# Kernel tuning notes

Hardware: AMD Instinct MI355X
Metric: run time of the kernel (lower is better)

Reference implementation:

```python
import jax, jax.numpy as jnp
import numpy as np

B, S, D = 4, 4096, 256


def setup_inputs() -> dict:
    key = jax.random.key(0)
    ks = jax.random.split(key, 8)
    scale = 1.0 / np.sqrt(D)
    inp = {
        "q": jax.random.normal(ks[0], (B, S, D), jnp.float32),
        "k": jax.random.normal(ks[1], (B, S, D), jnp.float32),
        "v": jax.random.normal(ks[2], (B, S, D), jnp.float32),
        # additive mask: 1 where attention is disallowed (causal), broadcast over batch
        "mask": jnp.triu(jnp.ones((S, S), jnp.float32), k=1)[None, :, :],
        "Wq": jax.random.normal(ks[3], (D, D), jnp.float32) * scale,
        "bq": jnp.zeros((D,), jnp.float32),
        "Wk": jax.random.normal(ks[4], (D, D), jnp.float32) * scale,
        "bk": jnp.zeros((D,), jnp.float32),
        "Wv": jax.random.normal(ks[5], (D, D), jnp.float32) * scale,
        "bv": jnp.zeros((D,), jnp.float32),
        "Wo": jax.random.normal(ks[6], (D, D), jnp.float32) * scale,
        "bo": jnp.zeros((D,), jnp.float32),
    }
    return inp


def reference(q, k, v, mask, Wq, bq, Wk, bk, Wv, bv, Wo, bo):
    # Dense projections (Keras Dense: x @ W + b)
    qp = q @ Wq + bq  # [B,S,D]
    kp = k @ Wk + bk
    vp = v @ Wv + bv
    dk = jnp.asarray(qp.shape[-1], qp.dtype)
    # scaled dot-product attention, materialized scores as in the source
    logits = jnp.einsum("bqd,bkd->bqk", qp, kp) / jnp.sqrt(dk)  # [B,S,S]
    logits = logits + mask * (-1e9)
    attn = jax.nn.softmax(logits, axis=-1)  # [B,S,S]
    ctx = jnp.einsum("bqk,bkd->bqd", attn, vp)  # [B,S,D]
    z = ctx @ Wo + bo
    return z, attn
```

## Files before the change

kernel.cpp:

```cpp
#include <hip/hip_runtime.h>


typedef unsigned short u16;
typedef __attribute__((ext_vector_type(8))) short short8;
typedef __attribute__((ext_vector_type(4))) float f32x4;

struct __align__(8) us4 { u16 x, y, z, w; };

#define SEQ 4096
#define DIM 256

__device__ __forceinline__ u16 f2bf(float f) {
  unsigned int u = __float_as_uint(f);
  u += 0x7fffu + ((u >> 16) & 1u);
  return (u16)(u >> 16);
}
__device__ __forceinline__ float bf2f(u16 u) {
  return __uint_as_float(((unsigned int)u) << 16);
}

__device__ __forceinline__ void cp16(const void* g, void* l) {
  __builtin_amdgcn_global_load_lds((const __attribute__((address_space(1))) void*)g,
                                   (__attribute__((address_space(3))) void*)l, 16, 0, 0);
}

__global__ void k_wt(const float* __restrict__ Wq, const float* __restrict__ Wk,
                     const float* __restrict__ Wv, const float* __restrict__ Wo,
                     u16* __restrict__ wt) {
  __shared__ float t[32][33];
  const float* W = blockIdx.z == 0 ? Wq : blockIdx.z == 1 ? Wk : blockIdx.z == 2 ? Wv : Wo;
  u16* out = wt + (size_t)blockIdx.z * 65536;
  int n0 = blockIdx.x * 32, k0 = blockIdx.y * 32;
  int tx = threadIdx.x, ty = threadIdx.y;
  for (int i = 0; i < 4; i++)
    t[ty + i * 8][tx] = W[(size_t)(k0 + ty + i * 8) * 256 + n0 + tx];
  __syncthreads();
  for (int i = 0; i < 4; i++)
    out[(size_t)(n0 + ty + i * 8) * 256 + k0 + tx] = f2bf(t[tx][ty + i * 8]);
}

__global__ void k_pgemm3(const float* __restrict__ qin, const float* __restrict__ kin,
                         const float* __restrict__ vin, const u16* __restrict__ wtall,
                         const float* __restrict__ bq, const float* __restrict__ bk,
                         const float* __restrict__ bv,
                         u16* __restrict__ qp, u16* __restrict__ kp,
                         u16* __restrict__ vpt) {
  __shared__ __align__(16) char smem[34816];
  const int z = blockIdx.z;
  const float* A = z == 0 ? qin : z == 1 ? kin : vin;
  const u16* Wt = wtall + (size_t)z * 65536;
  const float* bias = z == 0 ? bq : z == 1 ? bk : bv;
  u16* outp = z == 0 ? qp : z == 1 ? kp : vpt;
  const bool TRANS = (z == 2);

  u16* Asm = (u16*)smem;
  u16* Bsm = Asm + 4096;
  u16* tb = (u16*)smem;
  const int tid = threadIdx.x;
  const int lane = tid & 63, w = tid >> 6;
  const int wr = w >> 1, wc = w & 1;
  const int quad = lane >> 4, m16 = lane & 15;
  const int m0 = blockIdx.y * 128, n0 = blockIdx.x * 128;

  f32x4 zero = {0.f, 0.f, 0.f, 0.f};
  f32x4 acc[4][4];
  for (int i = 0; i < 4; i++)
    for (int j = 0; j < 4; j++) acc[i][j] = zero;

  for (int kk = 0; kk < 8; ++kk) {
    const int k0 = kk * 32;
    for (int h = 0; h < 2; ++h) {
      int c = tid + h * 256;
      int row = c >> 2, sub = c & 3;
      cp16(Wt + (size_t)(n0 + row) * 256 + k0 + sub * 8, Bsm + c * 8);
    }
    for (int h = 0; h < 4; ++h) {
      int idx = h * 256 + tid;
      int row = idx >> 3, q4 = idx & 7;
      float4 a4 = *(const float4*)(A + (size_t)(m0 + row) * 256 + k0 + q4 * 4);
      us4 o;
      o.x = f2bf(a4.x); o.y = f2bf(a4.y); o.z = f2bf(a4.z); o.w = f2bf(a4.w);
      *(us4*)(Asm + row * 32 + q4 * 4) = o;
    }
    __syncthreads();
    short8 a[4], b[4];
    for (int i = 0; i < 4; ++i)
      a[i] = *(const short8*)(Asm + (wr * 64 + i * 16 + m16) * 32 + quad * 8);
    for (int j = 0; j < 4; ++j)
      b[j] = *(const short8*)(Bsm + (wc * 64 + j * 16 + m16) * 32 + quad * 8);
    for (int i = 0; i < 4; ++i)
      for (int j = 0; j < 4; ++j)
        acc[i][j] = __builtin_amdgcn_mfma_f32_16x16x32_bf16(a[i], b[j], acc[i][j], 0, 0, 0);
    __syncthreads();
  }

  if (!TRANS) {
    for (int j = 0; j < 4; ++j) {
      int gn = n0 + wc * 64 + j * 16 + m16;
      float bvx = bias[gn];
      for (int i = 0; i < 4; ++i) {
        int gm = m0 + wr * 64 + i * 16 + quad * 4;
        for (int r = 0; r < 4; ++r)
          outp[(size_t)(gm + r) * 256 + gn] = f2bf(acc[i][j][r] + bvx);
      }
    }
  } else {
    for (int j = 0; j < 4; ++j) {
      int cn = wc * 64 + j * 16 + m16;
      float bvx = bias[n0 + cn];
      for (int i = 0; i < 4; ++i) {
        int rm = wr * 64 + i * 16 + quad * 4;
        us4 o;
        o.x = f2bf(acc[i][j][0] + bvx); o.y = f2bf(acc[i][j][1] + bvx);
        o.z = f2bf(acc[i][j][2] + bvx); o.w = f2bf(acc[i][j][3] + bvx);
        *(us4*)(tb + cn * 136 + rm) = o;
      }
    }
    __syncthreads();
    int b = m0 >> 12, s0 = m0 & 4095;
    u16* dst = outp + ((size_t)b << 20);
    for (int it = 0; it < 8; ++it) {
      int idx = it * 256 + tid;
      int n = idx >> 4, m8 = idx & 15;
      short8 v8 = *(const short8*)(tb + n * 136 + m8 * 8);
      *(short8*)(dst + (size_t)(n0 + n) * 4096 + s0 + m8 * 8) = v8;
    }
  }
}

__global__ void __launch_bounds__(256, 3) k_qk(const u16* __restrict__ qp,
                                               const u16* __restrict__ kp,
                                               u16* __restrict__ eb,
                                               float* __restrict__ attn,
                                               float* __restrict__ ps) {
  int lin = blockIdx.x + (blockIdx.y << 5) + (blockIdx.z << 10);
  int wid = (lin & 7) * 512 + (lin >> 3);
  const int kt = wid & 31, qt = (wid >> 5) & 31, bz = wid >> 10;
  const int tid = threadIdx.x;
  const int q0 = qt * 128, k0t = kt * 128;

  if (kt > qt) {
    float* attnb = attn + ((size_t)bz << 24);
    f32x4 z4 = {0.f, 0.f, 0.f, 0.f};
    for (int s = 0; s < 16; ++s) {
      int idx = tid + s * 256;
      int row = idx >> 5, c4 = idx & 31;
      __builtin_nontemporal_store(z4,
          (f32x4*)(attnb + (size_t)(q0 + row) * 4096 + k0t + c4 * 4));
    }
    return;
  }

  __shared__ __align__(16) char smem[34816];
  u16* A_lds = (u16*)smem;
  u16* B_lds = A_lds + 8192;
  u16* epi = (u16*)smem;
  __shared__ float prow[2][128];

  const int lane = tid & 63, w = tid >> 6;
  const int wr = w >> 1, wc = w & 1;
  const int quad = lane >> 4, m16 = lane & 15;
  const u16* Ab = qp + ((size_t)bz << 20);
  const u16* Bb = kp + ((size_t)bz << 20);

  short8 arg[4], brg[4];
  const int sc = tid & 7;
  int srow[4], soff[4];
  for (int t = 0; t < 4; ++t) {
    srow[t] = (t * 256 + tid) >> 3;
    soff[t] = srow[t] * 64 + ((((sc << 4) ^ ((srow[t] & 7) << 4))) >> 1);
  }

  auto stage_load = [&](int kk) {
    const int k0 = kk * 64;
    for (int t = 0; t < 4; ++t) {
      arg[t] = *(const short8*)(Ab + (size_t)(q0 + srow[t]) * 256 + k0 + sc * 8);
      brg[t] = *(const short8*)(Bb + (size_t)(k0t + srow[t]) * 256 + k0 + sc * 8);
    }
  };
  auto stage_write = [&]() {
    for (int t = 0; t < 4; ++t) {
      *(short8*)(A_lds + soff[t]) = arg[t];
      *(short8*)(B_lds + soff[t]) = brg[t];
    }
  };

  f32x4 zero = {0.f, 0.f, 0.f, 0.f};
  f32x4 acc[4][4];
  for (int i = 0; i < 4; i++)
    for (int j = 0; j < 4; j++) acc[i][j] = zero;

  stage_load(0);
  stage_write();
  __syncthreads();

  for (int kk = 0; kk < 4; ++kk) {
    if (kk + 1 < 4) stage_load(kk + 1);
    for (int ks = 0; ks < 2; ++ks) {
      short8 a[4], b[4];
      for (int i = 0; i < 4; ++i) {
        int row = wr * 64 + i * 16 + m16;
        int xb = (ks * 64 + quad * 16) ^ ((row & 7) << 4);
        a[i] = *(const short8*)(A_lds + row * 64 + (xb >> 1));
      }
      for (int j = 0; j < 4; ++j) {
        int n = wc * 64 + j * 16 + m16;
        int xb = (ks * 64 + quad * 16) ^ ((n & 7) << 4);
        b[j] = *(const short8*)(B_lds + n * 64 + (xb >> 1));
      }
      for (int i = 0; i < 4; ++i)
        for (int j = 0; j < 4; ++j)
          acc[i][j] = __builtin_amdgcn_mfma_f32_16x16x32_bf16(a[i], b[j], acc[i][j], 0, 0, 0);
    }
    __syncthreads();
    if (kk + 1 < 4) {
      stage_write();
      __syncthreads();
    }
  }

  float rs[4][4];
  for (int i = 0; i < 4; i++)
    for (int r = 0; r < 4; r++) rs[i][r] = 0.f;
  for (int i = 0; i < 4; ++i) {
    int gq = q0 + wr * 64 + i * 16 + quad * 4;
    for (int j = 0; j < 4; ++j) {
      int gk = k0t + wc * 64 + j * 16 + m16;
      for (int r = 0; r < 4; ++r) {
        float e = (gk <= gq + r) ? __expf(acc[i][j][r] * 0.0625f) : 0.f;
        acc[i][j][r] = e;
        rs[i][r] += e;
      }
    }
  }
  for (int off = 1; off < 16; off <<= 1)
    for (int i = 0; i < 4; ++i)
      for (int r = 0; r < 4; ++r) rs[i][r] += __shfl_xor(rs[i][r], off, 64);
  if (m16 == 0)
    for (int i = 0; i < 4; ++i)
      for (int r = 0; r < 4; ++r)
        prow[wc][wr * 64 + i * 16 + quad * 4 + r] = rs[i][r];

  for (int i = 0; i < 4; ++i)
    for (int j = 0; j < 4; ++j) {
      int rl = wr * 64 + i * 16 + quad * 4;
      int cl = wc * 64 + j * 16 + m16;
      for (int r = 0; r < 4; ++r) epi[(rl + r) * 136 + cl] = f2bf(acc[i][j][r]);
    }
  __syncthreads();

  u16* ebt = eb + ((size_t)bz * 528 + (size_t)(qt * (qt + 1) / 2 + kt)) * 16384;
  for (int it = 0; it < 8; ++it) {
    int idx = it * 256 + tid;
    int row = idx >> 4, m8 = idx & 15;
    short8 v8 = *(const short8*)(epi + row * 136 + m8 * 8);
    *(short8*)(ebt + row * 128 + m8 * 8) = v8;
  }
  if (tid < 128)
    ps[(size_t)(bz * 32 + kt) * 4096 + q0 + tid] = prow[0][tid] + prow[1][tid];
}

__global__ void __launch_bounds__(256) k_pv2(const u16* __restrict__ eb,
                                             const u16* __restrict__ vpt,
                                             const float* __restrict__ ps,
                                             float* __restrict__ attn,
                                             float* __restrict__ ctxf) {
  int lin = blockIdx.x + (blockIdx.y << 3) + (blockIdx.z << 8);
  int wid = (lin & 7) * 128 + (lin >> 3);
  const int nh = wid & 1, kg = (wid >> 1) & 3;
  const int qt = (wid >> 3) & 31, bz = wid >> 8;
  const int nt_lo = (kg * (qt + 1)) >> 2;
  const int nt_hi = ((kg + 1) * (qt + 1)) >> 2;
  if (nt_lo >= nt_hi) return;

  __shared__ u16 A_lds[2][128 * 64];
  __shared__ u16 B_lds[2][128 * 64];
  __shared__ float inv_lds[128];

  const int tid = threadIdx.x;
  const int lane = tid & 63, w = tid >> 6;
  const int wr = w >> 1, wc = w & 1;
  const int quad = lane >> 4, m16 = lane & 15;
  const int q0 = qt * 128;
  const u16* ebq = eb + ((size_t)bz * 528 + (size_t)(qt * (qt + 1) / 2)) * 16384;
  float* attnb = attn + ((size_t)bz << 24);
  const u16* vb = vpt + ((size_t)bz << 20) + (size_t)nh * 128 * 4096;

  if (tid < 128) {
    float s = 0.f;
    for (int kt = 0; kt <= qt; ++kt)
      s += ps[(size_t)(bz * 32 + kt) * 4096 + q0 + tid];
    inv_lds[tid] = 1.f / s;
  }

  short8 arg[4], brg[4];
  const int sc = tid & 7;
  int srow[4], soff[4];
  for (int t = 0; t < 4; ++t) {
    srow[t] = (t * 256 + tid) >> 3;
    soff[t] = srow[t] * 64 + ((((sc << 4) ^ ((srow[t] & 7) << 4))) >> 1);
  }

  auto stage_load = [&](int hh) {
    int t0 = nt_lo + (hh >> 1), h = hh & 1;
    const u16* tile = ebq + (size_t)t0 * 16384 + h * 64;
    int kt0 = t0 * 128 + h * 64;
    for (int t = 0; t < 4; ++t) {
      arg[t] = *(const short8*)(tile + srow[t] * 128 + sc * 8);
      brg[t] = *(const short8*)(vb + (size_t)srow[t] * 4096 + kt0 + sc * 8);
    }
  };
  auto stage_write = [&](int buf) {
    for (int t = 0; t < 4; ++t) {
      *(short8*)(A_lds[buf] + soff[t]) = arg[t];
      *(short8*)(B_lds[buf] + soff[t]) = brg[t];
    }
  };

  const int khalves = (nt_hi - nt_lo) * 2;
  stage_load(0);
  stage_write(0);
  __syncthreads();

  f32x4 zero = {0.f, 0.f, 0.f, 0.f};
  f32x4 acc[4][4];
  for (int i = 0; i < 4; i++)
    for (int j = 0; j < 4; j++) acc[i][j] = zero;

  for (int hh = 0; hh < khalves; ++hh) {
    const int buf = hh & 1;
    if (hh + 1 < khalves) stage_load(hh + 1);

    for (int p = 0; p < 4; ++p) {
      int idx = p * 256 + tid;
      int rl = idx >> 3, c8 = idx & 7;
      int lb = rl * 64 + ((((c8 << 4) ^ ((rl & 7) << 4))) >> 1);
      short8 e8 = *(const short8*)(A_lds[buf] + lb);
      float ivr = inv_lds[rl];
      f32x4 lo, hi;
      for (int t = 0; t < 4; ++t) lo[t] = bf2f((u16)e8[t]) * ivr;
      for (int t = 0; t < 4; ++t) hi[t] = bf2f((u16)e8[t + 4]) * ivr;
      int kcol = (nt_lo + (hh >> 1)) * 128 + (hh & 1) * 64 + (c8 << 3);
      float* dst = attnb + (size_t)(q0 + rl) * 4096 + kcol;
      __builtin_nontemporal_store(lo, (f32x4*)dst);
      __builtin_nontemporal_store(hi, (f32x4*)(dst + 4));
    }

    for (int ks = 0; ks < 2; ++ks) {
      short8 a[4], b[4];
      for (int i = 0; i < 4; ++i) {
        int row = wr * 64 + i * 16 + m16;
        int xb = (ks * 64 + quad * 16) ^ ((row & 7) << 4);
        a[i] = *(const short8*)(A_lds[buf] + row * 64 + (xb >> 1));
      }
      for (int j = 0; j < 4; ++j) {
        int n = wc * 64 + j * 16 + m16;
        int xb = (ks * 64 + quad * 16) ^ ((n & 7) << 4);
        b[j] = *(const short8*)(B_lds[buf] + n * 64 + (xb >> 1));
      }
      for (int i = 0; i < 4; ++i)
        for (int j = 0; j < 4; ++j)
          acc[i][j] = __builtin_amdgcn_mfma_f32_16x16x32_bf16(a[i], b[j], acc[i][j], 0, 0, 0);
    }

    if (hh + 1 < khalves) stage_write(buf ^ 1);
    __syncthreads();
  }

  float* ctxs = ctxf + ((size_t)(kg * 4 + bz) << 20);
  for (int i = 0; i < 4; ++i) {
    int rl = wr * 64 + i * 16 + quad * 4;
    for (int j = 0; j < 4; ++j) {
      int gn = nh * 128 + wc * 64 + j * 16 + m16;
      for (int r = 0; r < 4; ++r)
        ctxs[(size_t)(q0 + rl + r) * 256 + gn] = acc[i][j][r] * inv_lds[rl + r];
    }
  }
}

__global__ void k_cvt(const float* __restrict__ ctxf, u16* __restrict__ ctx) {
  size_t i4 = (size_t)blockIdx.x * 256 + threadIdx.x;
  int bz = (int)(i4 >> 18);
  size_t rem4 = i4 & (((size_t)1 << 18) - 1);
  int qrow = (int)(rem4 >> 6);
  int qt = qrow >> 7;
  const float4* base = (const float4*)ctxf;
  float4 s = make_float4(0.f, 0.f, 0.f, 0.f);
  for (int kg = 0; kg < 4; ++kg) {
    if ((((kg + 1) * (qt + 1)) >> 2) > ((kg * (qt + 1)) >> 2)) {
      float4 t = base[((size_t)(kg * 4 + bz) << 18) + rem4];
      s.x += t.x; s.y += t.y; s.z += t.z; s.w += t.w;
    }
  }
  us4 o;
  o.x = f2bf(s.x); o.y = f2bf(s.y); o.z = f2bf(s.z); o.w = f2bf(s.w);
  ((us4*)ctx)[i4] = o;
}

template <bool OUT_BF16>
__global__ void k_gemm(const u16* __restrict__ A, const u16* __restrict__ Wt,
                       const float* __restrict__ bias, void* __restrict__ outp) {
  __shared__ u16 Asm[128 * 32];
  __shared__ u16 Bsm[128 * 32];
  const int tid = threadIdx.x;
  const int lane = tid & 63, w = tid >> 6;
  const int wr = w >> 1, wc = w & 1;
  const int quad = lane >> 4, m16 = lane & 15;
  const int m0 = blockIdx.y * 128, n0 = blockIdx.x * 128;

  f32x4 zero = {0.f, 0.f, 0.f, 0.f};
  f32x4 acc[4][4];
  for (int i = 0; i < 4; i++)
    for (int j = 0; j < 4; j++) acc[i][j] = zero;

  for (int kk = 0; kk < 8; ++kk) {
    const int k0 = kk * 32;
    for (int h = 0; h < 2; ++h) {
      int c = tid + h * 256;
      int row = c >> 2, sub = c & 3;
      cp16(A + (size_t)(m0 + row) * 256 + k0 + sub * 8, Asm + c * 8);
      cp16(Wt + (size_t)(n0 + row) * 256 + k0 + sub * 8, Bsm + c * 8);
    }
    __syncthreads();
    short8 a[4], b[4];
    for (int i = 0; i < 4; ++i)
      a[i] = *(const short8*)(Asm + (wr * 64 + i * 16 + m16) * 32 + quad * 8);
    for (int j = 0; j < 4; ++j)
      b[j] = *(const short8*)(Bsm + (wc * 64 + j * 16 + m16) * 32 + quad * 8);
    for (int i = 0; i < 4; ++i)
      for (int j = 0; j < 4; ++j)
        acc[i][j] = __builtin_amdgcn_mfma_f32_16x16x32_bf16(a[i], b[j], acc[i][j], 0, 0, 0);
    __syncthreads();
  }

  for (int j = 0; j < 4; ++j) {
    int gn = n0 + wc * 64 + j * 16 + m16;
    float bv = bias[gn];
    for (int i = 0; i < 4; ++i) {
      int gm = m0 + wr * 64 + i * 16 + quad * 4;
      for (int r = 0; r < 4; ++r) {
        float val = acc[i][j][r] + bv;
        if (OUT_BF16)
          ((u16*)outp)[(size_t)(gm + r) * 256 + gn] = f2bf(val);
        else
          ((float*)outp)[(size_t)(gm + r) * 256 + gn] = val;
      }
    }
  }
}

extern "C" void kernel_launch(void* const* d_in, const int* in_sizes, int n_in,
                              void* d_out, int out_size, void* d_ws, size_t ws_size,
                              hipStream_t stream) {
  const float* q  = (const float*)d_in[0];
  const float* k  = (const float*)d_in[1];
  const float* v  = (const float*)d_in[2];
  const float* Wq = (const float*)d_in[4];
  const float* bq = (const float*)d_in[5];
  const float* Wk = (const float*)d_in[6];
  const float* bk = (const float*)d_in[7];
  const float* Wv = (const float*)d_in[8];
  const float* bv = (const float*)d_in[9];
  const float* Wo = (const float*)d_in[10];
  const float* bo = (const float*)d_in[11];

  const size_t MD = (size_t)16384 * 256;
  u16* qp  = (u16*)d_ws;
  u16* kp  = qp + MD;
  u16* vpt = kp + MD;
  u16* ctx = vpt + MD;
  u16* wt  = ctx + MD;
  float* ps   = (float*)(wt + 4 * 65536);
  float* ctxf = ps + (size_t)4 * 32 * 4096;
  u16* eb = (u16*)(ctxf + (size_t)16 * 1024 * 1024);

  float* zout = (float*)d_out;
  float* attn = zout + (size_t)4 * 4096 * 256;

  k_wt<<<dim3(8, 8, 4), dim3(32, 8), 0, stream>>>(Wq, Wk, Wv, Wo, wt);
  k_pgemm3<<<dim3(2, 128, 3), 256, 0, stream>>>(q, k, v, wt, bq, bk, bv, qp, kp, vpt);
  k_qk<<<dim3(32, 32, 4), 256, 0, stream>>>(qp, kp, eb, attn, ps);
  k_pv2<<<dim3(8, 32, 4), 256, 0, stream>>>(eb, vpt, ps, attn, ctxf);
  k_cvt<<<4096, 256, 0, stream>>>(ctxf, ctx);
  k_gemm<false><<<dim3(2, 128), 256, 0, stream>>>(ctx, wt + 3 * 65536, bo, zout);
}
```

Measured before the change: 494.6 us.

## Fuse split-K ctx reduction into output GEMM and store attn from registers

The separate k_cvt kernel that summed the split-K partial context buffers and converted them to bf16 is removed. The output projection GEMM now reads the fp32 partials directly, sums the active splits, converts to bf16 and writes the A tile into LDS, which saves a kernel launch and a bf16 round trip through global memory. Separately, in k_pv2 the normalized attention store now uses the staged global-load registers instead of re-reading LDS, which removes LDS reads from the inner loop. The GEMM A-tile load becomes synchronous register loads instead of async global-to-LDS copies, and each of the two N blocks repeats the reduction.

```diff
diff --git a/kernel.cpp b/kernel.cpp
--- a/kernel.cpp
+++ b/kernel.cpp
@@ -316,11 +316,24 @@
       *(short8*)(B_lds[buf] + soff[t]) = brg[t];
     }
   };
+  auto norm_store = [&](int hh) {
+    int kcol0 = (nt_lo + (hh >> 1)) * 128 + (hh & 1) * 64 + sc * 8;
+    for (int t = 0; t < 4; ++t) {
+      float ivr = inv_lds[srow[t]];
+      f32x4 lo, hi;
+      for (int u = 0; u < 4; ++u) lo[u] = bf2f((u16)arg[t][u]) * ivr;
+      for (int u = 0; u < 4; ++u) hi[u] = bf2f((u16)arg[t][u + 4]) * ivr;
+      float* dst = attnb + (size_t)(q0 + srow[t]) * 4096 + kcol0;
+      __builtin_nontemporal_store(lo, (f32x4*)dst);
+      __builtin_nontemporal_store(hi, (f32x4*)(dst + 4));
+    }
+  };
 
   const int khalves = (nt_hi - nt_lo) * 2;
   stage_load(0);
   stage_write(0);
   __syncthreads();
+  norm_store(0);
 
   f32x4 zero = {0.f, 0.f, 0.f, 0.f};
   f32x4 acc[4][4];
@@ -330,21 +343,6 @@
   for (int hh = 0; hh < khalves; ++hh) {
     const int buf = hh & 1;
     if (hh + 1 < khalves) stage_load(hh + 1);
-
-    for (int p = 0; p < 4; ++p) {
-      int idx = p * 256 + tid;
-      int rl = idx >> 3, c8 = idx & 7;
-      int lb = rl * 64 + ((((c8 << 4) ^ ((rl & 7) << 4))) >> 1);
-      short8 e8 = *(const short8*)(A_lds[buf] + lb);
-      float ivr = inv_lds[rl];
-      f32x4 lo, hi;
-      for (int t = 0; t < 4; ++t) lo[t] = bf2f((u16)e8[t]) * ivr;
-      for (int t = 0; t < 4; ++t) hi[t] = bf2f((u16)e8[t + 4]) * ivr;
-      int kcol = (nt_lo + (hh >> 1)) * 128 + (hh & 1) * 64 + (c8 << 3);
-      float* dst = attnb + (size_t)(q0 + rl) * 4096 + kcol;
-      __builtin_nontemporal_store(lo, (f32x4*)dst);
-      __builtin_nontemporal_store(hi, (f32x4*)(dst + 4));
-    }
 
     for (int ks = 0; ks < 2; ++ks) {
       short8 a[4], b[4];
@@ -363,7 +361,10 @@
           acc[i][j] = __builtin_amdgcn_mfma_f32_16x16x32_bf16(a[i], b[j], acc[i][j], 0, 0, 0);
     }
 
-    if (hh + 1 < khalves) stage_write(buf ^ 1);
+    if (hh + 1 < khalves) {
+      norm_store(hh + 1);
+      stage_write(buf ^ 1);
+    }
     __syncthreads();
   }
 
@@ -378,28 +379,8 @@
   }
 }
 
-__global__ void k_cvt(const float* __restrict__ ctxf, u16* __restrict__ ctx) {
-  size_t i4 = (size_t)blockIdx.x * 256 + threadIdx.x;
-  int bz = (int)(i4 >> 18);
-  size_t rem4 = i4 & (((size_t)1 << 18) - 1);
-  int qrow = (int)(rem4 >> 6);
-  int qt = qrow >> 7;
-  const float4* base = (const float4*)ctxf;
-  float4 s = make_float4(0.f, 0.f, 0.f, 0.f);
-  for (int kg = 0; kg < 4; ++kg) {
-    if ((((kg + 1) * (qt + 1)) >> 2) > ((kg * (qt + 1)) >> 2)) {
-      float4 t = base[((size_t)(kg * 4 + bz) << 18) + rem4];
-      s.x += t.x; s.y += t.y; s.z += t.z; s.w += t.w;
-    }
-  }
-  us4 o;
-  o.x = f2bf(s.x); o.y = f2bf(s.y); o.z = f2bf(s.z); o.w = f2bf(s.w);
-  ((us4*)ctx)[i4] = o;
-}
-
-template <bool OUT_BF16>
-__global__ void k_gemm(const u16* __restrict__ A, const u16* __restrict__ Wt,
-                       const float* __restrict__ bias, void* __restrict__ outp) {
+__global__ void k_gemm(const float* __restrict__ ctxf, const u16* __restrict__ Wt,
+                       const float* __restrict__ bias, float* __restrict__ outp) {
   __shared__ u16 Asm[128 * 32];
   __shared__ u16 Bsm[128 * 32];
   const int tid = threadIdx.x;
@@ -407,6 +388,12 @@
   const int wr = w >> 1, wc = w & 1;
   const int quad = lane >> 4, m16 = lane & 15;
   const int m0 = blockIdx.y * 128, n0 = blockIdx.x * 128;
+  const int bz = m0 >> 12, qrow0 = m0 & 4095;
+  const int qt = qrow0 >> 7;
+
+  bool act[4];
+  for (int kg = 0; kg < 4; ++kg)
+    act[kg] = (((kg + 1) * (qt + 1)) >> 2) > ((kg * (qt + 1)) >> 2);
 
   f32x4 zero = {0.f, 0.f, 0.f, 0.f};
   f32x4 acc[4][4];
@@ -418,8 +405,27 @@
     for (int h = 0; h < 2; ++h) {
       int c = tid + h * 256;
       int row = c >> 2, sub = c & 3;
-      cp16(A + (size_t)(m0 + row) * 256 + k0 + sub * 8, Asm + c * 8);
       cp16(Wt + (size_t)(n0 + row) * 256 + k0 + sub * 8, Bsm + c * 8);
+    }
+    for (int h = 0; h < 2; ++h) {
+      int idx = h * 256 + tid;
+      int row = idx >> 2, q8 = idx & 3;
+      size_t off = (size_t)(qrow0 + row) * 256 + k0 + q8 * 8;
+      float s[8] = {0.f, 0.f, 0.f, 0.f, 0.f, 0.f, 0.f, 0.f};
+      for (int kg = 0; kg < 4; ++kg) {
+        if (act[kg]) {
+          const float* p = ctxf + (((size_t)(kg * 4 + bz)) << 20) + off;
+          float4 a = *(const float4*)p;
+          float4 b = *(const float4*)(p + 4);
+          s[0] += a.x; s[1] += a.y; s[2] += a.z; s[3] += a.w;
+          s[4] += b.x; s[5] += b.y; s[6] += b.z; s[7] += b.w;
+        }
+      }
+      us4 o1, o2;
+      o1.x = f2bf(s[0]); o1.y = f2bf(s[1]); o1.z = f2bf(s[2]); o1.w = f2bf(s[3]);
+      o2.x = f2bf(s[4]); o2.y = f2bf(s[5]); o2.z = f2bf(s[6]); o2.w = f2bf(s[7]);
+      *(us4*)(Asm + row * 32 + q8 * 8) = o1;
+      *(us4*)(Asm + row * 32 + q8 * 8 + 4) = o2;
     }
     __syncthreads();
     short8 a[4], b[4];
@@ -438,13 +444,8 @@
     float bv = bias[gn];
     for (int i = 0; i < 4; ++i) {
       int gm = m0 + wr * 64 + i * 16 + quad * 4;
-      for (int r = 0; r < 4; ++r) {
-        float val = acc[i][j][r] + bv;
-        if (OUT_BF16)
-          ((u16*)outp)[(size_t)(gm + r) * 256 + gn] = f2bf(val);
-        else
-          ((float*)outp)[(size_t)(gm + r) * 256 + gn] = val;
-      }
+      for (int r = 0; r < 4; ++r)
+        outp[(size_t)(gm + r) * 256 + gn] = acc[i][j][r] + bv;
     }
   }
 }
@@ -468,8 +469,7 @@
   u16* qp  = (u16*)d_ws;
   u16* kp  = qp + MD;
   u16* vpt = kp + MD;
-  u16* ctx = vpt + MD;
-  u16* wt  = ctx + MD;
+  u16* wt  = vpt + MD;
   float* ps   = (float*)(wt + 4 * 65536);
   float* ctxf = ps + (size_t)4 * 32 * 4096;
   u16* eb = (u16*)(ctxf + (size_t)16 * 1024 * 1024);
@@ -481,6 +481,5 @@
   k_pgemm3<<<dim3(2, 128, 3), 256, 0, stream>>>(q, k, v, wt, bq, bk, bv, qp, kp, vpt);
   k_qk<<<dim3(32, 32, 4), 256, 0, stream>>>(qp, kp, eb, attn, ps);
   k_pv2<<<dim3(8, 32, 4), 256, 0, stream>>>(eb, vpt, ps, attn, ctxf);
-  k_cvt<<<4096, 256, 0, stream>>>(ctxf, ctx);
-  k_gemm<false><<<dim3(2, 128), 256, 0, stream>>>(ctx, wt + 3 * 65536, bo, zout);
-}
+  k_gemm<<<dim3(2, 128), 256, 0, stream>>>(ctxf, wt + 3 * 65536, bo, zout);
+}
```

Result: slower. 506.6 us (+2.4%).
